# Kernel optimization log

Hardware: AMD Instinct MI355X
Metric: run time of the kernel (lower is better)

The kernel has to match this reference:

```python
import jax, jax.numpy as jnp
import numpy as np

B, S, D = 4, 4096, 1024
EPS_LN = 1e-5
EPS_REC = 1e-8


def _layernorm(x, g, b):
    mu = jnp.mean(x, axis=-1, keepdims=True)
    var = jnp.mean((x - mu) ** 2, axis=-1, keepdims=True)
    return (x - mu) * jax.lax.rsqrt(var + EPS_LN) * g + b


def setup_inputs() -> dict:
    key = jax.random.key(0)
    ks = jax.random.split(key, 8)
    scale = 1.0 / np.sqrt(D)
    return {
        "x": jax.random.normal(ks[0], (B, S, D), dtype=jnp.float32),
        "x_prev": jax.random.normal(ks[1], (B, S, D), dtype=jnp.float32),
        "mu": jnp.float32(0.5),
        "decay_w": jax.random.uniform(ks[2], (D, 1), jnp.float32, -scale, scale),
        "decay_b": jnp.zeros((1,), jnp.float32),
        "ln1_g": jnp.ones((D,), jnp.float32),
        "ln1_b": jnp.zeros((D,), jnp.float32),
        "Wr_w": jax.random.uniform(ks[3], (D, D), jnp.float32, -scale, scale),
        "Wr_b": jnp.zeros((D,), jnp.float32),
        "Wv_w": jax.random.uniform(ks[4], (D, D), jnp.float32, -scale, scale),
        "Wv_b": jnp.zeros((D,), jnp.float32),
        "ln2_g": jnp.ones((D,), jnp.float32),
        "ln2_b": jnp.zeros((D,), jnp.float32),
    }


def reference(x, x_prev, mu, decay_w, decay_b, ln1_g, ln1_b,
              Wr_w, Wr_b, Wv_w, Wv_b, ln2_g, ln2_b):
    # Shift (token-mix by scalar mu)
    shifted = mu * x + (1.0 - mu) * x_prev  # [B,S,D]

    # SequenceMergingSeq with C = V = W = shifted
    decay = jax.nn.sigmoid(jnp.einsum("bsd,do->bso", shifted, decay_w) + decay_b)  # [B,S,1]
    e = jnp.exp(shifted)                       # [B,S,D]
    ea = jnp.sum(e, axis=-1, keepdims=True)    # [B,S,1]
    ev = e * shifted                           # [B,S,D]

    def step(carry, inp):
        a, b = carry
        d_t, ea_t, ev_t = inp
        a = d_t * a + ea_t            # [B,1]
        b = d_t * b + ev_t            # [B,D]
        return (a, b), b / (a + EPS_REC)

    init = (jnp.zeros((B, 1), shifted.dtype), jnp.zeros((B, D), shifted.dtype))
    xs = (jnp.swapaxes(decay, 0, 1), jnp.swapaxes(ea, 0, 1), jnp.swapaxes(ev, 0, 1))
    _, out_sbd = jax.lax.scan(step, init, xs)  # [S,B,D]
    merged = _layernorm(jnp.swapaxes(out_sbd, 0, 1), ln1_g, ln1_b)  # [B,S,D]

    # StateCoupling
    gate = jax.nn.sigmoid(jnp.einsum("bsd,ed->bse", merged, Wr_w) + Wr_b)
    value = jnp.einsum("bsd,ed->bse", merged, Wv_w) + Wv_b
    coupled = _layernorm(gate * value, ln2_g, ln2_b)

    return shifted + coupled
```

## Files before the change

### kernel.cpp

```cpp
#include <hip/hip_runtime.h>

#define BATCH 4
#define SEQ   4096
#define DIM   1024
#define NCH   512
#define CHK   8
#define NROWS (BATCH*SEQ)
#define NT    16

typedef __attribute__((ext_vector_type(4))) float f32x4;
typedef __attribute__((ext_vector_type(8))) short shortx8;
typedef __attribute__((ext_vector_type(4))) short shortx4;

static __device__ __forceinline__ unsigned short f2bf(float f){
    unsigned int u = __float_as_uint(f);
    u += 0x7FFFu + ((u >> 16) & 1u);
    return (unsigned short)(u >> 16);
}
static __device__ __forceinline__ float bf2f(unsigned short h){
    return __uint_as_float(((unsigned int)h) << 16);
}
static __device__ __forceinline__ float sigmoidf_fast(float x){
    return 1.0f / (1.0f + __expf(-x));
}
static __device__ __forceinline__ shortx4 pack4(f32x4 s){
    shortx4 o;
    o.x = (short)f2bf(s.x); o.y = (short)f2bf(s.y);
    o.z = (short)f2bf(s.z); o.w = (short)f2bf(s.w);
    return o;
}
static __device__ __forceinline__ f32x4 unpack4(shortx4 s){
    f32x4 o;
    o.x = bf2f((unsigned short)s.x); o.y = bf2f((unsigned short)s.y);
    o.z = bf2f((unsigned short)s.z); o.w = bf2f((unsigned short)s.w);
    return o;
}

__global__ __launch_bounds__(256) void k_pack_w(
    const float* __restrict__ Wr, const float* __restrict__ Wv,
    unsigned short* __restrict__ Wcat)
{
    const int n = blockIdx.x;
    const int grp = n >> 5, r = n & 31;
    const float* src = (r < 16) ? (Wr + (size_t)(grp*16 + r)*DIM)
                                : (Wv + (size_t)(grp*16 + (r-16))*DIM);
    const int tid = threadIdx.x;
    f32x4 v = reinterpret_cast<const f32x4*>(src)[tid];
    reinterpret_cast<shortx4*>(Wcat)[n*256 + tid] = pack4(v);
}

__global__ __launch_bounds__(256) void k_shift_scan(
    const float* __restrict__ X, const float* __restrict__ XP,
    const float* __restrict__ mu_p, const float* __restrict__ dw,
    const float* __restrict__ db_p,
    unsigned short* __restrict__ shifted,
    unsigned short* __restrict__ b_local, float* __restrict__ a_local,
    float* __restrict__ cumP)
{
    const int tid  = threadIdx.x;
    const int lane = tid & 63;
    const int wid  = tid >> 6;
    const int cid  = blockIdx.x*4 + wid;
    const int batch = cid >> 9;
    const int chunk = cid & (NCH-1);
    const int row0  = batch*SEQ + chunk*CHK;

    const float mu = mu_p[0];
    const float om = 1.0f - mu;
    const float db = db_p[0];

    const f32x4* dwv = reinterpret_cast<const f32x4*>(dw);
    const f32x4 w0 = dwv[lane], w1 = dwv[64+lane], w2 = dwv[128+lane], w3 = dwv[192+lane];

    f32x4 b0 = {0,0,0,0}, b1 = {0,0,0,0}, b2 = {0,0,0,0}, b3 = {0,0,0,0};
    float a_run = 0.f, cp = 1.f;

    const f32x4* Xv  = reinterpret_cast<const f32x4*>(X);
    const f32x4* XPv = reinterpret_cast<const f32x4*>(XP);
    shortx4* BL = reinterpret_cast<shortx4*>(b_local);
    shortx4* SH = reinterpret_cast<shortx4*>(shifted);

    for (int r = 0; r < CHK; ++r){
        const int row = row0 + r;
        const int rb  = row*(DIM/4);

        f32x4 x0 = Xv[rb+lane],     x1 = Xv[rb+64+lane],
              x2 = Xv[rb+128+lane], x3 = Xv[rb+192+lane];
        f32x4 p0 = XPv[rb+lane],     p1 = XPv[rb+64+lane],
              p2 = XPv[rb+128+lane], p3 = XPv[rb+192+lane];
        f32x4 s0 = mu*x0 + om*p0, s1 = mu*x1 + om*p1;
        f32x4 s2 = mu*x2 + om*p2, s3 = mu*x3 + om*p3;

        SH[rb+lane]     = pack4(s0);
        SH[rb+64+lane]  = pack4(s1);
        SH[rb+128+lane] = pack4(s2);
        SH[rb+192+lane] = pack4(s3);

        float dot = s0.x*w0.x + s0.y*w0.y + s0.z*w0.z + s0.w*w0.w
                  + s1.x*w1.x + s1.y*w1.y + s1.z*w1.z + s1.w*w1.w
                  + s2.x*w2.x + s2.y*w2.y + s2.z*w2.z + s2.w*w2.w
                  + s3.x*w3.x + s3.y*w3.y + s3.z*w3.z + s3.w*w3.w;

        f32x4 e0, e1, e2, e3;
        e0.x=__expf(s0.x); e0.y=__expf(s0.y); e0.z=__expf(s0.z); e0.w=__expf(s0.w);
        e1.x=__expf(s1.x); e1.y=__expf(s1.y); e1.z=__expf(s1.z); e1.w=__expf(s1.w);
        e2.x=__expf(s2.x); e2.y=__expf(s2.y); e2.z=__expf(s2.z); e2.w=__expf(s2.w);
        e3.x=__expf(s3.x); e3.y=__expf(s3.y); e3.z=__expf(s3.z); e3.w=__expf(s3.w);
        float ea = e0.x+e0.y+e0.z+e0.w + e1.x+e1.y+e1.z+e1.w
                 + e2.x+e2.y+e2.z+e2.w + e3.x+e3.y+e3.z+e3.w;

        #pragma unroll
        for (int off = 1; off < 64; off <<= 1){
            dot += __shfl_xor(dot, off, 64);
            ea  += __shfl_xor(ea,  off, 64);
        }

        const float dt = sigmoidf_fast(dot + db);
        a_run = dt*a_run + ea;
        cp   *= dt;
        b0 = dt*b0 + e0*s0;  b1 = dt*b1 + e1*s1;
        b2 = dt*b2 + e2*s2;  b3 = dt*b3 + e3*s3;

        BL[rb+lane]     = pack4(b0);
        BL[rb+64+lane]  = pack4(b1);
        BL[rb+128+lane] = pack4(b2);
        BL[rb+192+lane] = pack4(b3);
        if (lane == 0){ a_local[row] = a_run; cumP[row] = cp; }
    }
}

__global__ __launch_bounds__(256) void k_combine(
    const unsigned short* __restrict__ b_local, const float* __restrict__ a_local,
    const float* __restrict__ cumP,
    float* __restrict__ carryA, unsigned short* __restrict__ carryB)
{
    const int batch = blockIdx.x >> 2;
    const int dseg  = blockIdx.x & 3;
    const int d = dseg*256 + threadIdx.x;

    __shared__ float sP[NCH], sA[NCH];
    for (int c = threadIdx.x; c < NCH; c += 256){
        const int er = batch*SEQ + c*CHK + (CHK-1);
        sP[c] = cumP[er];
        sA[c] = a_local[er];
    }
    __syncthreads();

    const unsigned short* bl = b_local + (size_t)batch*SEQ*DIM;
    unsigned short* cB = carryB + (size_t)batch*NCH*DIM;
    const bool wA = (dseg == 0 && threadIdx.x == 0);

    float cb = 0.f, ca = 0.f;
    float f0 = bf2f(bl[(0*CHK+CHK-1)*DIM + d]);
    float f1 = bf2f(bl[(1*CHK+CHK-1)*DIM + d]);
    float f2 = bf2f(bl[(2*CHK+CHK-1)*DIM + d]);
    float f3 = bf2f(bl[(3*CHK+CHK-1)*DIM + d]);

    for (int c = 0; c < NCH; c += 4){
        const float v0=f0, v1=f1, v2=f2, v3=f3;
        if (c+4 < NCH){
            f0 = bf2f(bl[((c+4)*CHK+CHK-1)*DIM + d]);
            f1 = bf2f(bl[((c+5)*CHK+CHK-1)*DIM + d]);
            f2 = bf2f(bl[((c+6)*CHK+CHK-1)*DIM + d]);
            f3 = bf2f(bl[((c+7)*CHK+CHK-1)*DIM + d]);
        }
        cB[(c+0)*DIM + d] = f2bf(cb); if (wA) carryA[batch*NCH + c+0] = ca;
        cb = sP[c+0]*cb + v0;   ca = sP[c+0]*ca + sA[c+0];
        cB[(c+1)*DIM + d] = f2bf(cb); if (wA) carryA[batch*NCH + c+1] = ca;
        cb = sP[c+1]*cb + v1;   ca = sP[c+1]*ca + sA[c+1];
        cB[(c+2)*DIM + d] = f2bf(cb); if (wA) carryA[batch*NCH + c+2] = ca;
        cb = sP[c+2]*cb + v2;   ca = sP[c+2]*ca + sA[c+2];
        cB[(c+3)*DIM + d] = f2bf(cb); if (wA) carryA[batch*NCH + c+3] = ca;
        cb = sP[c+3]*cb + v3;   ca = sP[c+3]*ca + sA[c+3];
    }
}

static __device__ __forceinline__ void block_reduce2(float& s, float& s2, float* red, int tid){
    #pragma unroll
    for (int off = 1; off < 64; off <<= 1){
        s  += __shfl_xor(s,  off, 64);
        s2 += __shfl_xor(s2, off, 64);
    }
    const int wid = tid >> 6, lane = tid & 63;
    if (lane == 0){ red[wid] = s; red[4+wid] = s2; }
    __syncthreads();
    s  = red[0]+red[1]+red[2]+red[3];
    s2 = red[4]+red[5]+red[6]+red[7];
}

__global__ __launch_bounds__(256) void k_fix_ln1(
    const unsigned short* __restrict__ b_local, const float* __restrict__ a_local,
    const float* __restrict__ cumP, const float* __restrict__ carryA,
    const unsigned short* __restrict__ carryB,
    const float* __restrict__ g1, const float* __restrict__ bb1,
    unsigned short* __restrict__ merged)
{
    const int row = blockIdx.x;
    const int batch = row >> 12;
    const int t = row & (SEQ-1);
    const int c = t >> 3;
    const int tid = threadIdx.x;

    const float cpv = cumP[row];
    const float a = a_local[row] + cpv * carryA[batch*NCH + c];
    const float inv_a = 1.0f / (a + 1e-8f);

    f32x4 bl = unpack4(reinterpret_cast<const shortx4*>(b_local)[row*256 + tid]);
    f32x4 cb = unpack4(reinterpret_cast<const shortx4*>(carryB)[(batch*NCH + c)*256 + tid]);
    f32x4 o = (bl + cpv*cb) * inv_a;

    float s  = o.x+o.y+o.z+o.w;
    float s2 = o.x*o.x + o.y*o.y + o.z*o.z + o.w*o.w;
    __shared__ float red[8];
    block_reduce2(s, s2, red, tid);

    const float mean = s * (1.0f/DIM);
    const float rstd = rsqrtf(s2*(1.0f/DIM) - mean*mean + 1e-5f);
    f32x4 gg = reinterpret_cast<const f32x4*>(g1)[tid];
    f32x4 bb = reinterpret_cast<const f32x4*>(bb1)[tid];
    f32x4 m = (o - mean)*rstd*gg + bb;
    reinterpret_cast<shortx4*>(merged)[row*256 + tid] = pack4(m);
}

typedef __attribute__((address_space(3))) unsigned int lds_uint;
typedef __attribute__((address_space(1))) unsigned int glob_uint;
static __device__ __forceinline__ void gload16(const unsigned short* g, char* l){
    __builtin_amdgcn_global_load_lds((const glob_uint*)g, (lds_uint*)l, 16, 0, 0);
}
#define SBAR() do { __builtin_amdgcn_sched_barrier(0); __builtin_amdgcn_s_barrier(); __builtin_amdgcn_sched_barrier(0); } while(0)

__global__ __launch_bounds__(512, 2) void k_gemm(
    const unsigned short* __restrict__ A,
    const unsigned short* __restrict__ Bt,
    const float* __restrict__ rbias, const float* __restrict__ vbias,
    unsigned short* __restrict__ gv)
{
    __shared__ __align__(16) char lds[3*49152];
    const int tid  = threadIdx.x;
    const int lane = tid & 63;
    const int wid  = tid >> 6;
    const int wm   = wid >> 2;
    const int wn   = wid & 3;

    const int bid  = blockIdx.x;
    const int wgid = (bid & 7)*128 + (bid >> 3);
    const int mt = wgid >> 4, nt = wgid & 15;
    const int m0 = mt*256, n0 = nt*128;

    const int sr  = lane >> 2;
    const int scg = (lane & 3) ^ (((lane >> 5) & 1) << 1);
    const unsigned short* gA = A  + (size_t)(m0 + wid*16 + sr)*DIM + scg*8;
    const unsigned short* gB = Bt + (size_t)(n0 + wid*16 + sr)*DIM + scg*8;

    const int fr = lane & 15, fq = lane >> 4;
    const int soff = fr*64 + ((fq*16) ^ ((fr & 8) ? 32 : 0));

    f32x4 acc[8][2];
    #pragma unroll
    for (int i = 0; i < 8; ++i){ acc[i][0] = (f32x4){0,0,0,0}; acc[i][1] = (f32x4){0,0,0,0}; }

    auto STAGE_A = [&](int buf, int tk){
        char* dst = &lds[buf*49152 + wid*2048];
        const unsigned short* src = gA + tk*64;
        gload16(src,             dst);
        gload16(src + 32,        dst + 1024);
        gload16(src + 128*DIM,      dst + 16384);
        gload16(src + 128*DIM + 32, dst + 16384 + 1024);
    };
    auto STAGE_B = [&](int buf, int tk){
        char* dst = &lds[buf*49152 + 32768 + wid*2048];
        const unsigned short* src = gB + tk*64;
        gload16(src,      dst);
        gload16(src + 32, dst + 1024);
    };

    STAGE_A(0, 0); STAGE_B(0, 0);
    STAGE_A(1, 1); STAGE_B(1, 1);
    asm volatile("s_waitcnt vmcnt(6)" ::: "memory");
    SBAR();

    int bc = 0, bn = 2;
    for (int t = 0; t < NT; ++t){
        const char* bufA = &lds[bc*49152];
        const char* bufB = bufA + 32768;

        shortx8 bq[2][2], af[4][2];
        #pragma unroll
        for (int nf = 0; nf < 2; ++nf)
            #pragma unroll
            for (int ks = 0; ks < 2; ++ks)
                bq[nf][ks] = *reinterpret_cast<const shortx8*>(bufB + ((wn*2+nf)*2+ks)*1024 + soff);
        #pragma unroll
        for (int mf = 0; mf < 4; ++mf)
            #pragma unroll
            for (int ks = 0; ks < 2; ++ks)
                af[mf][ks] = *reinterpret_cast<const shortx8*>(bufA + wm*16384 + (mf*2+ks)*1024 + soff);
        if (t < NT-2) STAGE_A(bn, t+2);
        SBAR();
        __builtin_amdgcn_s_setprio(1);
        #pragma unroll
        for (int mf = 0; mf < 4; ++mf)
            #pragma unroll
            for (int nf = 0; nf < 2; ++nf){
                acc[mf][nf] = __builtin_amdgcn_mfma_f32_16x16x32_bf16(af[mf][0], bq[nf][0], acc[mf][nf], 0,0,0);
                acc[mf][nf] = __builtin_amdgcn_mfma_f32_16x16x32_bf16(af[mf][1], bq[nf][1], acc[mf][nf], 0,0,0);
            }
        __builtin_amdgcn_s_setprio(0);
        SBAR();

        #pragma unroll
        for (int mf = 0; mf < 4; ++mf)
            #pragma unroll
            for (int ks = 0; ks < 2; ++ks)
                af[mf][ks] = *reinterpret_cast<const shortx8*>(bufA + wm*16384 + ((mf+4)*2+ks)*1024 + soff);
        if (t < NT-2){
            STAGE_B(bn, t+2);
            asm volatile("s_waitcnt vmcnt(6)" ::: "memory");
        } else {
            asm volatile("s_waitcnt vmcnt(0)" ::: "memory");
        }
        SBAR();
        __builtin_amdgcn_s_setprio(1);
        #pragma unroll
        for (int mf = 0; mf < 4; ++mf)
            #pragma unroll
            for (int nf = 0; nf < 2; ++nf){
                acc[mf+4][nf] = __builtin_amdgcn_mfma_f32_16x16x32_bf16(af[mf][0], bq[nf][0], acc[mf+4][nf], 0,0,0);
                acc[mf+4][nf] = __builtin_amdgcn_mfma_f32_16x16x32_bf16(af[mf][1], bq[nf][1], acc[mf+4][nf], 0,0,0);
            }
        __builtin_amdgcn_s_setprio(0);
        SBAR();

        bc = (bc == 2) ? 0 : bc+1;
        bn = (bn == 2) ? 0 : bn+1;
    }

    __syncthreads();
    unsigned short* ep = reinterpret_cast<unsigned short*>(lds);
    const int e = (nt*4 + wn)*16 + fr;
    const float rbe = rbias[e], vbe = vbias[e];
    #pragma unroll
    for (int mf = 0; mf < 8; ++mf){
        const int rbase = wm*128 + mf*16 + fq*4;
        #pragma unroll
        for (int q = 0; q < 4; ++q){
            const float g = sigmoidf_fast(acc[mf][0][q] + rbe);
            const float v = acc[mf][1][q] + vbe;
            ep[(rbase + q)*64 + wn*16 + fr] = f2bf(g*v);
        }
    }
    __syncthreads();
    #pragma unroll
    for (int p = 0; p < 4; ++p){
        const int row = p*64 + (tid >> 3);
        const int cg8 = tid & 7;
        shortx8 val = *reinterpret_cast<const shortx8*>(&ep[row*64 + cg8*8]);
        *reinterpret_cast<shortx8*>(&gv[(size_t)(m0+row)*DIM + nt*64 + cg8*8]) = val;
    }
}

__global__ __launch_bounds__(256) void k_ln2_res(
    const unsigned short* __restrict__ gvb, const unsigned short* __restrict__ shifted,
    const float* __restrict__ g2, const float* __restrict__ b2,
    float* __restrict__ out)
{
    const int row = blockIdx.x, tid = threadIdx.x;
    const int idx = row*256 + tid;
    f32x4 v = unpack4(reinterpret_cast<const shortx4*>(gvb)[idx]);
    float s  = v.x+v.y+v.z+v.w;
    float s2 = v.x*v.x + v.y*v.y + v.z*v.z + v.w*v.w;
    __shared__ float red[8];
    block_reduce2(s, s2, red, tid);
    const float mean = s * (1.0f/DIM);
    const float rstd = rsqrtf(s2*(1.0f/DIM) - mean*mean + 1e-5f);
    f32x4 gg = reinterpret_cast<const f32x4*>(g2)[tid];
    f32x4 bb = reinterpret_cast<const f32x4*>(b2)[tid];
    f32x4 nv = (v - mean)*rstd*gg + bb;
    f32x4 sh = unpack4(reinterpret_cast<const shortx4*>(shifted)[idx]);
    reinterpret_cast<f32x4*>(out)[idx] = sh + nv;
}

extern "C" void kernel_launch(void* const* d_in, const int* in_sizes, int n_in,
                              void* d_out, int out_size, void* d_ws, size_t ws_size,
                              hipStream_t stream)
{
    (void)in_sizes; (void)n_in; (void)out_size; (void)ws_size;
    const float* x     = (const float*)d_in[0];
    const float* xprev = (const float*)d_in[1];
    const float* mu    = (const float*)d_in[2];
    const float* dw    = (const float*)d_in[3];
    const float* db    = (const float*)d_in[4];
    const float* ln1g  = (const float*)d_in[5];
    const float* ln1b  = (const float*)d_in[6];
    const float* Wr    = (const float*)d_in[7];
    const float* Wrb   = (const float*)d_in[8];
    const float* Wv    = (const float*)d_in[9];
    const float* Wvb   = (const float*)d_in[10];
    const float* ln2g  = (const float*)d_in[11];
    const float* ln2b  = (const float*)d_in[12];
    float* out = (float*)d_out;

    char* ws = (char*)d_ws;
    size_t off = 0;
    auto alloc = [&](size_t bytes) -> void* {
        void* p = ws + off;
        off += (bytes + 255) & ~(size_t)255;
        return p;
    };
    unsigned short* shifted = (unsigned short*)alloc((size_t)NROWS*DIM*2);
    unsigned short* b_local = (unsigned short*)alloc((size_t)NROWS*DIM*2);
    unsigned short* merged  = (unsigned short*)alloc((size_t)NROWS*DIM*2);
    unsigned short* carryB  = (unsigned short*)alloc((size_t)BATCH*NCH*DIM*2);
    unsigned short* Wcat    = (unsigned short*)alloc((size_t)2048*1024*2);
    float* a_local          = (float*)alloc((size_t)NROWS*4);
    float* cumP             = (float*)alloc((size_t)NROWS*4);
    float* carryA           = (float*)alloc((size_t)BATCH*NCH*4);
    unsigned short* gvbuf   = b_local;

    hipLaunchKernelGGL(k_pack_w,    dim3(2048),  dim3(256), 0, stream, Wr, Wv, Wcat);
    hipLaunchKernelGGL(k_shift_scan,dim3(512),   dim3(256), 0, stream,
                       x, xprev, mu, dw, db, shifted, b_local, a_local, cumP);
    hipLaunchKernelGGL(k_combine,   dim3(16),    dim3(256), 0, stream,
                       b_local, a_local, cumP, carryA, carryB);
    hipLaunchKernelGGL(k_fix_ln1,   dim3(16384), dim3(256), 0, stream,
                       b_local, a_local, cumP, carryA, carryB, ln1g, ln1b, merged);
    hipLaunchKernelGGL(k_gemm,      dim3(1024),  dim3(512), 0, stream,
                       merged, Wcat, Wrb, Wvb, gvbuf);
    hipLaunchKernelGGL(k_ln2_res,   dim3(16384), dim3(256), 0, stream,
                       gvbuf, shifted, ln2g, ln2b, out);
}
```

Before: 236.9 us.

## Enlarge GEMM tile to 256x256 with K=32 steps and 4-stage LDS pipeline

The gate/value GEMM now uses 256x256 output tiles (512 blocks instead of 1024), with each wave computing 4x8 MFMA fragments. K is split into 32-wide steps across a 4-buffer LDS ring that prefetches three tiles ahead. The epilogue writes through a padded LDS stride before storing. The goal is to raise arithmetic intensity and cut redundant A/B loads, at the cost of more accumulator registers, a larger 128KB LDS footprint that may limit occupancy, and fewer blocks than CUs for load balance.

```diff
diff --git a/kernel.cpp b/kernel.cpp
--- a/kernel.cpp
+++ b/kernel.cpp
@@ -6,7 +6,7 @@
 #define NCH   512
 #define CHK   8
 #define NROWS (BATCH*SEQ)
-#define NT    16
+#define NKT   32
 
 typedef __attribute__((ext_vector_type(4))) float f32x4;
 typedef __attribute__((ext_vector_type(8))) short shortx8;
@@ -228,6 +228,7 @@
     __builtin_amdgcn_global_load_lds((const glob_uint*)g, (lds_uint*)l, 16, 0, 0);
 }
 #define SBAR() do { __builtin_amdgcn_sched_barrier(0); __builtin_amdgcn_s_barrier(); __builtin_amdgcn_sched_barrier(0); } while(0)
+#define LDSE 136
 
 __global__ __launch_bounds__(512, 2) void k_gemm(
     const unsigned short* __restrict__ A,
@@ -235,7 +236,7 @@
     const float* __restrict__ rbias, const float* __restrict__ vbias,
     unsigned short* __restrict__ gv)
 {
-    __shared__ __align__(16) char lds[3*49152];
+    __shared__ __align__(16) char lds[131072];
     const int tid  = threadIdx.x;
     const int lane = tid & 63;
     const int wid  = tid >> 6;
@@ -243,119 +244,112 @@
     const int wn   = wid & 3;
 
     const int bid  = blockIdx.x;
-    const int wgid = (bid & 7)*128 + (bid >> 3);
-    const int mt = wgid >> 4, nt = wgid & 15;
-    const int m0 = mt*256, n0 = nt*128;
+    const int wgid = (bid & 7)*64 + (bid >> 3);
+    const int mt = wgid >> 3, nt = wgid & 7;
+    const int m0 = mt*256, n0 = nt*256;
 
     const int sr  = lane >> 2;
-    const int scg = (lane & 3) ^ (((lane >> 5) & 1) << 1);
-    const unsigned short* gA = A  + (size_t)(m0 + wid*16 + sr)*DIM + scg*8;
-    const unsigned short* gB = Bt + (size_t)(n0 + wid*16 + sr)*DIM + scg*8;
+    const int scg = (lane & 3) ^ ((lane >> 5) << 1);
+    const unsigned short* gA = A  + (size_t)(m0 + wid*32 + sr)*DIM + scg*8;
+    const unsigned short* gB = Bt + (size_t)(n0 + wid*32 + sr)*DIM + scg*8;
 
     const int fr = lane & 15, fq = lane >> 4;
     const int soff = fr*64 + ((fq*16) ^ ((fr & 8) ? 32 : 0));
 
-    f32x4 acc[8][2];
+    f32x4 acc[8][4];
     #pragma unroll
-    for (int i = 0; i < 8; ++i){ acc[i][0] = (f32x4){0,0,0,0}; acc[i][1] = (f32x4){0,0,0,0}; }
-
-    auto STAGE_A = [&](int buf, int tk){
-        char* dst = &lds[buf*49152 + wid*2048];
-        const unsigned short* src = gA + tk*64;
-        gload16(src,             dst);
-        gload16(src + 32,        dst + 1024);
-        gload16(src + 128*DIM,      dst + 16384);
-        gload16(src + 128*DIM + 32, dst + 16384 + 1024);
+    for (int i = 0; i < 8; ++i)
+        #pragma unroll
+        for (int j = 0; j < 4; ++j) acc[i][j] = (f32x4){0,0,0,0};
+
+    auto STAGE_A = [&](int tk){
+        char* dst = &lds[(tk & 3)*32768 + wid*2048];
+        const unsigned short* s0 = gA + tk*32;
+        gload16(s0,          dst);
+        gload16(s0 + 16*DIM, dst + 1024);
     };
-    auto STAGE_B = [&](int buf, int tk){
-        char* dst = &lds[buf*49152 + 32768 + wid*2048];
-        const unsigned short* src = gB + tk*64;
-        gload16(src,      dst);
-        gload16(src + 32, dst + 1024);
+    auto STAGE_B = [&](int tk){
+        char* dst = &lds[(tk & 3)*32768 + 16384 + wid*2048];
+        const unsigned short* s0 = gB + tk*32;
+        gload16(s0,          dst);
+        gload16(s0 + 16*DIM, dst + 1024);
     };
 
-    STAGE_A(0, 0); STAGE_B(0, 0);
-    STAGE_A(1, 1); STAGE_B(1, 1);
-    asm volatile("s_waitcnt vmcnt(6)" ::: "memory");
+    STAGE_A(0); STAGE_B(0);
+    STAGE_A(1); STAGE_B(1);
+    STAGE_A(2); STAGE_B(2);
+    asm volatile("s_waitcnt vmcnt(8)" ::: "memory");
     SBAR();
 
-    int bc = 0, bn = 2;
-    for (int t = 0; t < NT; ++t){
-        const char* bufA = &lds[bc*49152];
-        const char* bufB = bufA + 32768;
-
-        shortx8 bq[2][2], af[4][2];
-        #pragma unroll
-        for (int nf = 0; nf < 2; ++nf)
-            #pragma unroll
-            for (int ks = 0; ks < 2; ++ks)
-                bq[nf][ks] = *reinterpret_cast<const shortx8*>(bufB + ((wn*2+nf)*2+ks)*1024 + soff);
+    for (int t = 0; t < NKT; ++t){
+        const char* bufA = &lds[(t & 3)*32768];
+        const char* bufB = bufA + 16384;
+        shortx8 af[4], bf[4];
+
+        #pragma unroll
+        for (int mf = 0; mf < 4; ++mf)
+            af[mf] = *reinterpret_cast<const shortx8*>(bufA + (wm*8 + mf)*1024 + soff);
+        #pragma unroll
+        for (int nf = 0; nf < 4; ++nf)
+            bf[nf] = *reinterpret_cast<const shortx8*>(bufB + (wn*4 + nf)*1024 + soff);
+        if (t + 3 < NKT) STAGE_A(t + 3);
+        SBAR();
+        asm volatile("s_waitcnt lgkmcnt(0)" ::: "memory");
+        __builtin_amdgcn_sched_barrier(0);
+        __builtin_amdgcn_s_setprio(1);
         #pragma unroll
         for (int mf = 0; mf < 4; ++mf)
             #pragma unroll
-            for (int ks = 0; ks < 2; ++ks)
-                af[mf][ks] = *reinterpret_cast<const shortx8*>(bufA + wm*16384 + (mf*2+ks)*1024 + soff);
-        if (t < NT-2) STAGE_A(bn, t+2);
+            for (int nf = 0; nf < 4; ++nf)
+                acc[mf][nf] = __builtin_amdgcn_mfma_f32_16x16x32_bf16(af[mf], bf[nf], acc[mf][nf], 0, 0, 0);
+        __builtin_amdgcn_s_setprio(0);
         SBAR();
+
+        #pragma unroll
+        for (int mf = 0; mf < 4; ++mf)
+            af[mf] = *reinterpret_cast<const shortx8*>(bufA + (wm*8 + mf + 4)*1024 + soff);
+        if (t + 3 < NKT) STAGE_B(t + 3);
+        if (t <= NKT - 4)      asm volatile("s_waitcnt vmcnt(8)" ::: "memory");
+        else if (t == NKT - 3) asm volatile("s_waitcnt vmcnt(4)" ::: "memory");
+        else                   asm volatile("s_waitcnt vmcnt(0)" ::: "memory");
+        SBAR();
+        asm volatile("s_waitcnt lgkmcnt(0)" ::: "memory");
+        __builtin_amdgcn_sched_barrier(0);
         __builtin_amdgcn_s_setprio(1);
         #pragma unroll
         for (int mf = 0; mf < 4; ++mf)
             #pragma unroll
-            for (int nf = 0; nf < 2; ++nf){
-                acc[mf][nf] = __builtin_amdgcn_mfma_f32_16x16x32_bf16(af[mf][0], bq[nf][0], acc[mf][nf], 0,0,0);
-                acc[mf][nf] = __builtin_amdgcn_mfma_f32_16x16x32_bf16(af[mf][1], bq[nf][1], acc[mf][nf], 0,0,0);
-            }
+            for (int nf = 0; nf < 4; ++nf)
+                acc[mf+4][nf] = __builtin_amdgcn_mfma_f32_16x16x32_bf16(af[mf], bf[nf], acc[mf+4][nf], 0, 0, 0);
         __builtin_amdgcn_s_setprio(0);
         SBAR();
-
-        #pragma unroll
-        for (int mf = 0; mf < 4; ++mf)
-            #pragma unroll
-            for (int ks = 0; ks < 2; ++ks)
-                af[mf][ks] = *reinterpret_cast<const shortx8*>(bufA + wm*16384 + ((mf+4)*2+ks)*1024 + soff);
-        if (t < NT-2){
-            STAGE_B(bn, t+2);
-            asm volatile("s_waitcnt vmcnt(6)" ::: "memory");
-        } else {
-            asm volatile("s_waitcnt vmcnt(0)" ::: "memory");
-        }
-        SBAR();
-        __builtin_amdgcn_s_setprio(1);
-        #pragma unroll
-        for (int mf = 0; mf < 4; ++mf)
-            #pragma unroll
-            for (int nf = 0; nf < 2; ++nf){
-                acc[mf+4][nf] = __builtin_amdgcn_mfma_f32_16x16x32_bf16(af[mf][0], bq[nf][0], acc[mf+4][nf], 0,0,0);
-                acc[mf+4][nf] = __builtin_amdgcn_mfma_f32_16x16x32_bf16(af[mf][1], bq[nf][1], acc[mf+4][nf], 0,0,0);
-            }
-        __builtin_amdgcn_s_setprio(0);
-        SBAR();
-
-        bc = (bc == 2) ? 0 : bc+1;
-        bn = (bn == 2) ? 0 : bn+1;
     }
 
     __syncthreads();
     unsigned short* ep = reinterpret_cast<unsigned short*>(lds);
-    const int e = (nt*4 + wn)*16 + fr;
-    const float rbe = rbias[e], vbe = vbias[e];
     #pragma unroll
-    for (int mf = 0; mf < 8; ++mf){
-        const int rbase = wm*128 + mf*16 + fq*4;
-        #pragma unroll
-        for (int q = 0; q < 4; ++q){
-            const float g = sigmoidf_fast(acc[mf][0][q] + rbe);
-            const float v = acc[mf][1][q] + vbe;
-            ep[(rbase + q)*64 + wn*16 + fr] = f2bf(g*v);
+    for (int pr = 0; pr < 2; ++pr){
+        const int el = wn*32 + pr*16 + fr;
+        const float rbe = rbias[nt*128 + el];
+        const float vbe = vbias[nt*128 + el];
+        #pragma unroll
+        for (int mf = 0; mf < 8; ++mf){
+            const int rbase = wm*128 + mf*16 + fq*4;
+            f32x4 ga = acc[mf][2*pr], va = acc[mf][2*pr+1];
+            #pragma unroll
+            for (int q = 0; q < 4; ++q){
+                const float g = sigmoidf_fast(ga[q] + rbe);
+                ep[(rbase + q)*LDSE + el] = f2bf(g*(va[q] + vbe));
+            }
         }
     }
     __syncthreads();
     #pragma unroll
-    for (int p = 0; p < 4; ++p){
-        const int row = p*64 + (tid >> 3);
-        const int cg8 = tid & 7;
-        shortx8 val = *reinterpret_cast<const shortx8*>(&ep[row*64 + cg8*8]);
-        *reinterpret_cast<shortx8*>(&gv[(size_t)(m0+row)*DIM + nt*64 + cg8*8]) = val;
+    for (int p = 0; p < 8; ++p){
+        const int r  = p*32 + (tid >> 4);
+        const int c8 = tid & 15;
+        shortx8 val = *reinterpret_cast<const shortx8*>(&ep[r*LDSE + c8*8]);
+        *reinterpret_cast<shortx8*>(&gv[(size_t)(m0 + r)*DIM + nt*128 + c8*8]) = val;
     }
 }
 
@@ -424,7 +418,7 @@
                        b_local, a_local, cumP, carryA, carryB);
     hipLaunchKernelGGL(k_fix_ln1,   dim3(16384), dim3(256), 0, stream,
                        b_local, a_local, cumP, carryA, carryB, ln1g, ln1b, merged);
-    hipLaunchKernelGGL(k_gemm,      dim3(1024),  dim3(512), 0, stream,
+    hipLaunchKernelGGL(k_gemm,      dim3(512),   dim3(512), 0, stream,
                        merged, Wcat, Wrb, Wvb, gvbuf);
     hipLaunchKernelGGL(k_ln2_res,   dim3(16384), dim3(256), 0, stream,
                        gvbuf, shifted, ln2g, ln2b, out);
```

Measured after the change: 230.8 us. 1.03x faster.
